# Performance work log

Measured on AMD Instinct MI355X. Metric: run time of the kernel, lower is better.

The kernel has to match this reference:

```python
import jax, jax.numpy as jnp
import numpy as np

EPS = 1e-3  # keras BatchNormalization default epsilon
NUM_HEADS = 8


def conv1d_same(x, w, b):
    # x: [B,T,Cin], w: [K,Cin,Cout]
    return jax.lax.conv_general_dilated(
        x, w, window_strides=(1,), padding='SAME',
        dimension_numbers=('NWC', 'WIO', 'NWC')) + b


def bn(x, g, b, m, v):
    # inference-mode batchnorm with moving stats
    return (x - m) * jax.lax.rsqrt(v + EPS) * g + b


def lstm(x, K, R, b):
    # x: [B,T,D] -> [B,T,U]; keras gate order i,f,c,o; recurrent_dropout off at inference
    B = x.shape[0]
    U = R.shape[0]
    xp = jnp.einsum('btd,dz->btz', x, K) + b  # precompute input projection

    def step(carry, xt):
        h, c = carry
        z = xt + h @ R
        i, f, g, o = jnp.split(z, 4, axis=-1)
        c = jax.nn.sigmoid(f) * c + jax.nn.sigmoid(i) * jnp.tanh(g)
        h = jax.nn.sigmoid(o) * jnp.tanh(c)
        return (h, c), h

    h0 = jnp.zeros((B, U), x.dtype)
    _, hs = jax.lax.scan(step, (h0, h0), jnp.swapaxes(xp, 0, 1))
    return jnp.swapaxes(hs, 0, 1)


def bilstm(x, Kf, Rf, bf, Kb, Rb, bb):
    fwd = lstm(x, Kf, Rf, bf)
    bwd = lstm(x[:, ::-1], Kb, Rb, bb)[:, ::-1]
    return jnp.concatenate([fwd, bwd], axis=-1)


def mhsa(x, wq, bq, wk, bk, wv, bv, wo, bo):
    B, T, _ = x.shape
    d_model = wq.shape[1]
    dh = d_model // NUM_HEADS
    q = (x @ wq + bq).reshape(B, T, NUM_HEADS, dh)
    k = (x @ wk + bk).reshape(B, T, NUM_HEADS, dh)
    v = (x @ wv + bv).reshape(B, T, NUM_HEADS, dh)
    logits = jnp.einsum('bqhd,bkhd->bhqk', q, k) / jnp.sqrt(jnp.asarray(dh, x.dtype))
    attn = jax.nn.softmax(logits, axis=-1)
    out = jnp.einsum('bhqk,bkhd->bqhd', attn, v).reshape(B, T, d_model)
    return out @ wo + bo


def setup_inputs() -> dict:
    key = jax.random.key(0)
    ks = iter(jax.random.split(key, 64))

    def nrm(shape, s=0.05):
        return (jax.random.normal(next(ks), shape) * s).astype(jnp.float32)

    p = {}
    p['x'] = jax.random.normal(next(ks), (512, 256, 78), dtype=jnp.float32)
    for name, shp in [
            ('conv5_w', (5, 78, 64)), ('conv7_w', (7, 78, 64)), ('conv9_w', (9, 78, 64)),
            ('fuse_w', (1, 192, 128)), ('se_w1', (128, 8)), ('se_w2', (8, 128)),
            ('l1f_k', (128, 512)), ('l1f_r', (128, 512)), ('l1b_k', (128, 512)), ('l1b_r', (128, 512)),
            ('l2f_k', (256, 256)), ('l2f_r', (64, 256)), ('l2b_k', (256, 256)), ('l2b_r', (64, 256)),
            ('wq', (128, 256)), ('wk', (128, 256)), ('wv', (128, 256)), ('wo', (256, 256)),
            ('d1_w', (256, 256)), ('d2_w', (256, 128)), ('d3_w', (128, 1)),
            ('conv5_b', (64,)), ('conv7_b', (64,)), ('conv9_b', (64,)), ('fuse_b', (128,)),
            ('se_b1', (8,)), ('se_b2', (128,)),
            ('l1f_b', (512,)), ('l1b_b', (512,)), ('l2f_b', (256,)), ('l2b_b', (256,)),
            ('bq', (256,)), ('bk', (256,)), ('bv', (256,)), ('bo', (256,)),
            ('d1_b', (256,)), ('d2_b', (128,)), ('d3_b', (1,))]:
        p[name] = nrm(shp)
    for tag, c in [('bn5', 64), ('bn7', 64), ('bn9', 64), ('bn_l1', 256),
                   ('bn_l2', 128), ('bn_d1', 256), ('bn_d2', 128)]:
        p[tag + '_g'] = jnp.ones((c,), jnp.float32)
        p[tag + '_b'] = jnp.zeros((c,), jnp.float32)
        p[tag + '_m'] = jnp.zeros((c,), jnp.float32)
        p[tag + '_v'] = jnp.ones((c,), jnp.float32)
    return p


def reference(x, conv5_w, conv5_b, bn5_g, bn5_b, bn5_m, bn5_v,
              conv7_w, conv7_b, bn7_g, bn7_b, bn7_m, bn7_v,
              conv9_w, conv9_b, bn9_g, bn9_b, bn9_m, bn9_v,
              fuse_w, fuse_b, se_w1, se_b1, se_w2, se_b2,
              l1f_k, l1f_r, l1f_b, l1b_k, l1b_r, l1b_b,
              bn_l1_g, bn_l1_b, bn_l1_m, bn_l1_v,
              l2f_k, l2f_r, l2f_b, l2b_k, l2b_r, l2b_b,
              bn_l2_g, bn_l2_b, bn_l2_m, bn_l2_v,
              wq, bq, wk, bk, wv, bv, wo, bo,
              d1_w, d1_b, bn_d1_g, bn_d1_b, bn_d1_m, bn_d1_v,
              d2_w, d2_b, bn_d2_g, bn_d2_b, bn_d2_m, bn_d2_v,
              d3_w, d3_b):
    def block(w, b, g, bt, m, v):
        h = jax.nn.relu(conv1d_same(x, w, b))
        h = bn(h, g, bt, m, v)
        B, T, C = h.shape  # MaxPooling1D(2, 'same'); T is even
        return h.reshape(B, T // 2, 2, C).max(axis=2)

    fused = jnp.concatenate([
        block(conv5_w, conv5_b, bn5_g, bn5_b, bn5_m, bn5_v),
        block(conv7_w, conv7_b, bn7_g, bn7_b, bn7_m, bn7_v),
        block(conv9_w, conv9_b, bn9_g, bn9_b, bn9_m, bn9_v)], axis=-1)
    fused = conv1d_same(fused, fuse_w, fuse_b)

    # SENet spatial attention
    s = fused.mean(axis=1)
    e = jax.nn.sigmoid(jax.nn.relu(s @ se_w1 + se_b1) @ se_w2 + se_b2)
    h = fused * e[:, None, :]

    h = bilstm(h, l1f_k, l1f_r, l1f_b, l1b_k, l1b_r, l1b_b)
    h = bn(h, bn_l1_g, bn_l1_b, bn_l1_m, bn_l1_v)
    h = bilstm(h, l2f_k, l2f_r, l2f_b, l2b_k, l2b_r, l2b_b)
    h = bn(h, bn_l2_g, bn_l2_b, bn_l2_m, bn_l2_v)

    h = mhsa(h, wq, bq, wk, bk, wv, bv, wo, bo)
    g_ = h.mean(axis=1)

    d = jax.nn.relu(g_ @ d1_w + d1_b)
    d = bn(d, bn_d1_g, bn_d1_b, bn_d1_m, bn_d1_v)
    d = jax.nn.relu(d @ d2_w + d2_b)
    d = bn(d, bn_d2_g, bn_d2_b, bn_d2_m, bn_d2_v)
    return jax.nn.sigmoid(d @ d3_w + d3_b)
```

## Files before the change

### kernel.cpp

```cpp
#include <hip/hip_runtime.h>

#define EPS 1e-3f

typedef __attribute__((ext_vector_type(8))) short bf16x8;
typedef __attribute__((ext_vector_type(4))) float f32x4;

__device__ __forceinline__ float sigm(float x){ return 1.0f/(1.0f + __expf(-x)); }
__device__ __forceinline__ float tanhfast(float x){ return 1.0f - 2.0f/(1.0f + __expf(2.0f*x)); }

__device__ __forceinline__ unsigned short f2b(float f){
    union { float f; unsigned u; } v; v.f = f;
    unsigned r = v.u + 0x7FFFu + ((v.u >> 16) & 1u);
    return (unsigned short)(r >> 16);
}
__device__ __forceinline__ float b2f(unsigned short h){
    union { unsigned u; float f; } v; v.u = ((unsigned)h) << 16; return v.f;
}

__global__ void __launch_bounds__(256)
prep_x(const float* __restrict__ x, unsigned short* __restrict__ xbf)
{
    const int b = blockIdx.x;
    const float* xs = x + (size_t)b*256*78;
    unsigned short* xd = xbf + (size_t)b*264*96;
    for (int p = threadIdx.x; p < 264*48; p += 256){
        int row = p / 48;
        int cp  = (p - row*48) * 2;
        int t   = row - 4;
        unsigned short v0 = 0, v1 = 0;
        if (t >= 0 && t < 256){
            if (cp   < 78) v0 = f2b(xs[t*78 + cp]);
            if (cp+1 < 78) v1 = f2b(xs[t*78 + cp + 1]);
        }
        *(unsigned int*)(xd + row*96 + cp) = (unsigned)v0 | ((unsigned)v1 << 16);
    }
}

__global__ void __launch_bounds__(256)
prep_w(const float* __restrict__ w5, const float* __restrict__ w7, const float* __restrict__ w9,
       unsigned short* __restrict__ wfrag)
{
    int g = blockIdx.x*256 + threadIdx.x;
    if (g >= 27*12*64) return;
    union { unsigned short s[8]; uint4 v; } u;
    int base = g * 8;
    #pragma unroll
    for (int e = 0; e < 8; ++e){
        int lin  = base + e;
        int slot = lin & 511;
        int fi   = lin >> 9;
        int nt   = fi % 12, kcs = fi / 12;
        int k    = kcs / 3, cs = kcs - k*3;
        int l15  = slot >> 5, r = slot & 31;
        int lg   = r >> 3, ee = r & 7;
        int ci   = cs*32 + lg*8 + ee;
        int co   = nt*16 + l15;
        float val = 0.f;
        if (ci < 78){
            if (co < 64){
                int kk = k - 2;
                if (kk >= 0 && kk < 5) val = w5[(kk*78 + ci)*64 + co];
            } else if (co < 128){
                int kk = k - 1;
                if (kk >= 0 && kk < 7) val = w7[(kk*78 + ci)*64 + (co - 64)];
            } else {
                val = w9[(k*78 + ci)*64 + (co - 128)];
            }
        }
        u.s[e] = f2b(val);
    }
    *(uint4*)(wfrag + base) = u.v;
}

__global__ void prep_ss(const float* b5, const float* b7, const float* b9,
                        const float* g5, const float* be5, const float* m5, const float* v5,
                        const float* g7, const float* be7, const float* m7, const float* v7,
                        const float* g9, const float* be9, const float* m9, const float* v9,
                        float* __restrict__ biascat, float* __restrict__ scale, float* __restrict__ shift)
{
    int c = threadIdx.x;
    if (c >= 192) return;
    float bv, g, be, m, v;
    if (c < 64){        bv=b5[c];      g=g5[c];      be=be5[c];      m=m5[c];      v=v5[c]; }
    else if (c < 128){  int i=c-64;  bv=b7[i]; g=g7[i]; be=be7[i]; m=m7[i]; v=v7[i]; }
    else {              int i=c-128; bv=b9[i]; g=g9[i]; be=be9[i]; m=m9[i]; v=v9[i]; }
    float s = g * rsqrtf(v + EPS);
    biascat[c] = bv;
    scale[c]   = s;
    shift[c]   = be - m*s;
}

__global__ void __launch_bounds__(256)
conv_mfma(const unsigned short* __restrict__ xbf,
          const unsigned short* __restrict__ wfrag,
          const float* __restrict__ biascat, const float* __restrict__ scale,
          const float* __restrict__ shift,
          float* __restrict__ out)
{
    const int b = blockIdx.x, tile = blockIdx.y;
    const int tid = threadIdx.x, lane = tid & 63, wv = tid >> 6;
    const int l15 = lane & 15, lg = lane >> 4;
    const int nt0 = wv * 3;
    const int t0  = tile * 64;

    f32x4 acc[4][3];
    #pragma unroll
    for (int nt = 0; nt < 3; ++nt){
        float bv = biascat[(nt0 + nt)*16 + l15];
        #pragma unroll
        for (int mt = 0; mt < 4; ++mt)
            acc[mt][nt] = (f32x4){bv, bv, bv, bv};
    }

    const unsigned short* xb = xbf + ((size_t)b*264 + t0 + l15)*96 + lg*8;
    const unsigned short* wb = wfrag + (size_t)nt0*512 + l15*32 + lg*8;

    for (int k = 0; k < 9; ++k){
        #pragma unroll
        for (int cs = 0; cs < 3; ++cs){
            bf16x8 A[4], Bf[3];
            #pragma unroll
            for (int mt = 0; mt < 4; ++mt)
                A[mt] = *(const bf16x8*)(xb + (size_t)(k + mt*16)*96 + cs*32);
            #pragma unroll
            for (int nt = 0; nt < 3; ++nt)
                Bf[nt] = *(const bf16x8*)(wb + (size_t)((k*3 + cs)*12 + nt)*512);
            #pragma unroll
            for (int mt = 0; mt < 4; ++mt)
                #pragma unroll
                for (int nt = 0; nt < 3; ++nt)
                    acc[mt][nt] = __builtin_amdgcn_mfma_f32_16x16x32_bf16(A[mt], Bf[nt], acc[mt][nt], 0, 0, 0);
        }
    }

    #pragma unroll
    for (int nt = 0; nt < 3; ++nt){
        int col = (nt0 + nt)*16 + l15;
        float s = scale[col], sh = shift[col];
        #pragma unroll
        for (int mt = 0; mt < 4; ++mt){
            float v0 = fmaxf(acc[mt][nt][0], 0.f)*s + sh;
            float v1 = fmaxf(acc[mt][nt][1], 0.f)*s + sh;
            float v2 = fmaxf(acc[mt][nt][2], 0.f)*s + sh;
            float v3 = fmaxf(acc[mt][nt][3], 0.f)*s + sh;
            int tb = tile*32 + mt*8 + lg*2;
            out[((size_t)b*128 + tb    )*192 + col] = fmaxf(v0, v1);
            out[((size_t)b*128 + tb + 1)*192 + col] = fmaxf(v2, v3);
        }
    }
}

__global__ void __launch_bounds__(128)
se_mean(const unsigned short* __restrict__ fb,
        const float* __restrict__ w1, const float* __restrict__ b1,
        const float* __restrict__ w2, const float* __restrict__ b2,
        float* __restrict__ e)
{
    int b = blockIdx.x, c = threadIdx.x;
    __shared__ float sv[128];
    __shared__ float rv[8];
    const unsigned short* fp = fb + (size_t)b*128*128 + c;
    float acc = 0.f;
    for (int t = 0; t < 128; ++t) acc += b2f(fp[t*128]);
    sv[c] = acc * (1.f/128.f);
    __syncthreads();
    if (c < 8){
        float r = b1[c];
        for (int i = 0; i < 128; ++i) r = fmaf(sv[i], w1[i*8 + c], r);
        rv[c] = fmaxf(r, 0.f);
    }
    __syncthreads();
    float ev = b2[c];
    #pragma unroll
    for (int j = 0; j < 8; ++j) ev = fmaf(rv[j], w2[j*128 + c], ev);
    e[(size_t)b*128 + c] = sigm(ev);
}

template<int K, bool ABF16, int OUTMODE, bool ESCALE>
__global__ void __launch_bounds__(256)
xp_gemm(const void* __restrict__ Av, const float* __restrict__ W,
        const float* __restrict__ bias, const float* __restrict__ esc,
        unsigned short* __restrict__ outp, int N)
{
    __shared__ unsigned short Asm[128][40];
    __shared__ unsigned short Bsm[8][64][8];
    __shared__ float esm[ESCALE ? K : 1];

    const int tid  = threadIdx.x;
    const int lane = tid & 63;
    const int wv   = tid >> 6;
    const int wm   = wv & 1;
    const int wn   = wv >> 1;
    const size_t m0 = (size_t)blockIdx.x * 128;
    const int n0   = blockIdx.y * 128;

    if constexpr (ESCALE){
        for (int i = tid; i < K; i += 256) esm[i] = esc[(size_t)blockIdx.x*K + i];
    }

    f32x4 acc[4][4];
    #pragma unroll
    for (int nt = 0; nt < 4; ++nt){
        float bv = bias[n0 + wn*64 + nt*16 + (lane & 15)];
        #pragma unroll
        for (int mt = 0; mt < 4; ++mt)
            acc[mt][nt] = (f32x4){bv, bv, bv, bv};
    }

    const int bn = tid & 127;
    const int bg = tid >> 7;

    for (int k0 = 0; k0 < K; k0 += 32){
        __syncthreads();
        if constexpr (!ABF16){
            const float* Ag = (const float*)Av;
            #pragma unroll
            for (int i = 0; i < 2; ++i){
                int g = tid + i*256;
                int r = g >> 2, c8 = g & 3;
                float4 d0 = *(const float4*)(Ag + (m0 + r)*K + k0 + c8*8);
                float4 d1 = *(const float4*)(Ag + (m0 + r)*K + k0 + c8*8 + 4);
                union { unsigned short s[8]; uint4 v; } u;
                u.s[0]=f2b(d0.x); u.s[1]=f2b(d0.y); u.s[2]=f2b(d0.z); u.s[3]=f2b(d0.w);
                u.s[4]=f2b(d1.x); u.s[5]=f2b(d1.y); u.s[6]=f2b(d1.z); u.s[7]=f2b(d1.w);
                *(uint4*)&Asm[r][c8*8] = u.v;
            }
        } else {
            const unsigned short* Ag = (const unsigned short*)Av;
            #pragma unroll
            for (int i = 0; i < 2; ++i){
                int g = tid + i*256;
                int r = g >> 2, c8 = g & 3;
                uint4 d = *(const uint4*)(Ag + (m0 + r)*K + k0 + c8*8);
                if constexpr (ESCALE){
                    unsigned short* s = (unsigned short*)&d;
                    #pragma unroll
                    for (int j = 0; j < 8; ++j)
                        s[j] = f2b(b2f(s[j]) * esm[k0 + c8*8 + j]);
                }
                *(uint4*)&Asm[r][c8*8] = d;
            }
        }
        {
            union { unsigned short s[8]; uint4 v; } u0, u1;
            #pragma unroll
            for (int q = 0; q < 8; ++q){
                u0.s[q] = f2b(W[(size_t)(k0 + bg*16 + q)*N + n0 + bn]);
                u1.s[q] = f2b(W[(size_t)(k0 + bg*16 + 8 + q)*N + n0 + bn]);
            }
            int nt = bn >> 4, lo = bn & 15;
            *(uint4*)&Bsm[nt][lo + 16*(2*bg)][0]   = u0.v;
            *(uint4*)&Bsm[nt][lo + 16*(2*bg+1)][0] = u1.v;
        }
        __syncthreads();

        bf16x8 af[4], bfr[4];
        #pragma unroll
        for (int mt = 0; mt < 4; ++mt)
            af[mt] = *(const bf16x8*)&Asm[wm*64 + mt*16 + (lane & 15)][(lane >> 4)*8];
        #pragma unroll
        for (int nt = 0; nt < 4; ++nt)
            bfr[nt] = *(const bf16x8*)&Bsm[wn*4 + nt][lane][0];
        #pragma unroll
        for (int mt = 0; mt < 4; ++mt)
            #pragma unroll
            for (int nt = 0; nt < 4; ++nt)
                acc[mt][nt] = __builtin_amdgcn_mfma_f32_16x16x32_bf16(af[mt], bfr[nt], acc[mt][nt], 0, 0, 0);
    }

    #pragma unroll
    for (int mt = 0; mt < 4; ++mt)
        #pragma unroll
        for (int nt = 0; nt < 4; ++nt)
            #pragma unroll
            for (int r = 0; r < 4; ++r){
                size_t row = m0 + wm*64 + mt*16 + (lane >> 4)*4 + r;
                int    col = n0 + wn*64 + nt*16 + (lane & 15);
                if constexpr (OUTMODE == 0){
                    outp[row*N + col] = f2b(acc[mt][nt][r]);
                } else if constexpr (OUTMODE == 1){
                    size_t off = ((size_t)((row >> 7)*8 + (col >> 5))*32 + (col & 31))*128 + (row & 127);
                    outp[off] = f2b(acc[mt][nt][r]);
                } else {
                    const int U = N/4;
                    outp[row*N + (col & (U-1))*4 + (col / U)] = f2b(acc[mt][nt][r]);
                }
            }
}

template<int U>
__global__ void __launch_bounds__(4*U)
lstm_rec5(const unsigned short* __restrict__ xpf, const unsigned short* __restrict__ xpb,
          const float* __restrict__ Rf, const float* __restrict__ Rb,
          const float* __restrict__ bng, const float* __restrict__ bnb,
          const float* __restrict__ bnm, const float* __restrict__ bnv,
          unsigned short* __restrict__ outv)
{
    constexpr int Z  = 4*U;
    constexpr int KT = U/32;
    constexpr int HP = U + 8;

    __shared__ unsigned short h_lds[2][16][HP];

    const int tid = threadIdx.x, lane = tid & 63, wv = tid >> 6;
    const int l15 = lane & 15, lg = lane >> 4;
    const int dir = blockIdx.y;
    const int b0  = blockIdx.x * 16;

    const unsigned short* xp = dir ? xpb : xpf;
    const float* Rg = dir ? Rb : Rf;

    for (int i = tid; i < 2*16*HP; i += 4*U) ((unsigned short*)h_lds)[i] = 0;

    bf16x8 rf[KT][4];
    #pragma unroll
    for (int kt = 0; kt < KT; ++kt)
        #pragma unroll
        for (int g = 0; g < 4; ++g){
            union { unsigned short s[8]; bf16x8 v; } u;
            #pragma unroll
            for (int e = 0; e < 8; ++e)
                u.s[e] = f2b(Rg[(size_t)(kt*32 + lg*8 + e)*Z + g*U + wv*16 + l15]);
            rf[kt][g] = u.v;
        }

    const int u_ = wv*16 + l15;
    const int ch = dir*U + u_;
    const float bns  = bng[ch] * rsqrtf(bnv[ch] + EPS);
    const float bnsh = bnb[ch] - bnm[ch]*bns;
    float cst[4] = {0.f, 0.f, 0.f, 0.f};
    const unsigned short* xbase = xp + ((size_t)(b0 + lg*4)*128)*Z + u_*4;

    ushort4 xq[4];
    {
        const int tf = dir ? 127 : 0;
        #pragma unroll
        for (int r = 0; r < 4; ++r)
            xq[r] = *(const ushort4*)(xbase + ((size_t)r*128 + tf)*Z);
    }
    __syncthreads();

    int buf = 0;
    for (int ts = 0; ts < 128; ++ts){
        const int t = dir ? 127 - ts : ts;
        ushort4 xn[4] = {};
        if (ts < 127){
            const int tn = dir ? t - 1 : t + 1;
            #pragma unroll
            for (int r = 0; r < 4; ++r)
                xn[r] = *(const ushort4*)(xbase + ((size_t)r*128 + tn)*Z);
        }
        bf16x8 af[KT];
        #pragma unroll
        for (int kt = 0; kt < KT; ++kt)
            af[kt] = *(const bf16x8*)&h_lds[buf][l15][kt*32 + lg*8];
        f32x4 acc[4];
        #pragma unroll
        for (int g = 0; g < 4; ++g) acc[g] = (f32x4){0.f,0.f,0.f,0.f};
        #pragma unroll
        for (int kt = 0; kt < KT; ++kt)
            #pragma unroll
            for (int g = 0; g < 4; ++g)
                acc[g] = __builtin_amdgcn_mfma_f32_16x16x32_bf16(af[kt], rf[kt][g], acc[g], 0, 0, 0);
        #pragma unroll
        for (int r = 0; r < 4; ++r){
            float zi = acc[0][r] + b2f(xq[r].x);
            float zf = acc[1][r] + b2f(xq[r].y);
            float zg = acc[2][r] + b2f(xq[r].z);
            float zo = acc[3][r] + b2f(xq[r].w);
            float c  = sigm(zf)*cst[r] + sigm(zi)*tanhfast(zg);
            cst[r] = c;
            float h = sigm(zo)*tanhfast(c);
            h_lds[buf^1][lg*4 + r][u_] = f2b(h);
            size_t oidx = ((size_t)(b0 + lg*4 + r)*128 + t)*(size_t)(2*U) + ch;
            outv[oidx] = f2b(fmaf(h, bns, bnsh));
        }
        asm volatile("s_waitcnt lgkmcnt(0)" ::: "memory");
        __builtin_amdgcn_s_barrier();
        buf ^= 1;
        #pragma unroll
        for (int r = 0; r < 4; ++r) xq[r] = xn[r];
    }
}

__global__ void __launch_bounds__(256)
attn_kernel(const unsigned short* __restrict__ qb,
            const unsigned short* __restrict__ kb,
            const unsigned short* __restrict__ vb,
            float* __restrict__ msum)
{
    __shared__ unsigned short p_lds[128][136];
    __shared__ float red[4][2][16];

    const int b  = blockIdx.x, hd = blockIdx.y;
    const int tid = threadIdx.x, lane = tid & 63, wv = tid >> 6;
    const int m0 = wv * 32;
    const int l15 = lane & 15, lg = lane >> 4;

    bf16x8 aq[2];
    #pragma unroll
    for (int mt = 0; mt < 2; ++mt)
        aq[mt] = *(const bf16x8*)(qb + ((size_t)(b*128 + m0 + mt*16 + l15))*256 + hd*32 + lg*8);

    bf16x8 bk[8];
    #pragma unroll
    for (int nt = 0; nt < 8; ++nt)
        bk[nt] = *(const bf16x8*)(kb + ((size_t)(b*128 + nt*16 + l15))*256 + hd*32 + lg*8);

    f32x4 s[2][8];
    #pragma unroll
    for (int mt = 0; mt < 2; ++mt)
        #pragma unroll
        for (int nt = 0; nt < 8; ++nt) s[mt][nt] = (f32x4){0.f,0.f,0.f,0.f};
    #pragma unroll
    for (int mt = 0; mt < 2; ++mt)
        #pragma unroll
        for (int nt = 0; nt < 8; ++nt)
            s[mt][nt] = __builtin_amdgcn_mfma_f32_16x16x32_bf16(aq[mt], bk[nt], s[mt][nt], 0, 0, 0);

    const float scale = 0.17677669529663687f;
    #pragma unroll
    for (int mt = 0; mt < 2; ++mt)
        #pragma unroll
        for (int r = 0; r < 4; ++r){
            float mx = -1e30f;
            #pragma unroll
            for (int nt = 0; nt < 8; ++nt) mx = fmaxf(mx, s[mt][nt][r]);
            #pragma unroll
            for (int msk = 1; msk < 16; msk <<= 1) mx = fmaxf(mx, __shfl_xor(mx, msk, 64));
            float pv[8], sum = 0.f;
            #pragma unroll
            for (int nt = 0; nt < 8; ++nt){
                pv[nt] = __expf((s[mt][nt][r] - mx) * scale);
                sum += pv[nt];
            }
            #pragma unroll
            for (int msk = 1; msk < 16; msk <<= 1) sum += __shfl_xor(sum, msk, 64);
            float inv = 1.f / sum;
            int row = m0 + mt*16 + lg*4 + r;
            #pragma unroll
            for (int nt = 0; nt < 8; ++nt)
                p_lds[row][nt*16 + l15] = f2b(pv[nt] * inv);
        }
    __syncthreads();

    f32x4 o[2][2];
    #pragma unroll
    for (int mt = 0; mt < 2; ++mt)
        #pragma unroll
        for (int dn = 0; dn < 2; ++dn) o[mt][dn] = (f32x4){0.f,0.f,0.f,0.f};
    bf16x8 bv[4][2];
    #pragma unroll
    for (int kt = 0; kt < 4; ++kt)
        #pragma unroll
        for (int dn = 0; dn < 2; ++dn)
            bv[kt][dn] = *(const bf16x8*)(vb + ((size_t)(b*8 + hd)*32 + dn*16 + l15)*128 + kt*32 + lg*8);
    #pragma unroll
    for (int mt = 0; mt < 2; ++mt)
        #pragma unroll
        for (int kt = 0; kt < 4; ++kt){
            bf16x8 ap = *(const bf16x8*)&p_lds[m0 + mt*16 + l15][kt*32 + lg*8];
            #pragma unroll
            for (int dn = 0; dn < 2; ++dn)
                o[mt][dn] = __builtin_amdgcn_mfma_f32_16x16x32_bf16(ap, bv[kt][dn], o[mt][dn], 0, 0, 0);
        }

    float sm[2];
    #pragma unroll
    for (int dn = 0; dn < 2; ++dn){
        float a = 0.f;
        #pragma unroll
        for (int mt = 0; mt < 2; ++mt)
            #pragma unroll
            for (int r = 0; r < 4; ++r) a += o[mt][dn][r];
        a += __shfl_xor(a, 16, 64);
        a += __shfl_xor(a, 32, 64);
        sm[dn] = a;
    }
    if (lg == 0){
        red[wv][0][l15] = sm[0];
        red[wv][1][l15] = sm[1];
    }
    __syncthreads();
    if (tid < 32){
        int dn = tid >> 4, n = tid & 15;
        float tot = red[0][dn][n] + red[1][dn][n] + red[2][dn][n] + red[3][dn][n];
        msum[(size_t)b*256 + hd*32 + dn*16 + n] = tot * (1.f/128.f);
    }
}

__global__ void __launch_bounds__(256)
head_kernel(const float* __restrict__ msum,
            const float* __restrict__ wo, const float* __restrict__ bo,
            const float* __restrict__ d1w, const float* __restrict__ d1b,
            const float* __restrict__ g1, const float* __restrict__ b1,
            const float* __restrict__ m1, const float* __restrict__ v1,
            const float* __restrict__ d2w, const float* __restrict__ d2b,
            const float* __restrict__ g2, const float* __restrict__ b2,
            const float* __restrict__ m2, const float* __restrict__ v2,
            const float* __restrict__ d3w, const float* __restrict__ d3b,
            float* __restrict__ outp)
{
    int b = blockIdx.x, j = threadIdx.x;
    __shared__ float s1[256];
    __shared__ float s2[256];
    const float* mr = msum + (size_t)b*256;
    float acc = bo[j];
    #pragma unroll 4
    for (int i = 0; i < 256; ++i) acc = fmaf(mr[i], wo[i*256 + j], acc);
    s1[j] = acc;
    __syncthreads();
    float a1 = d1b[j];
    #pragma unroll 4
    for (int i = 0; i < 256; ++i) a1 = fmaf(s1[i], d1w[i*256 + j], a1);
    a1 = fmaxf(a1, 0.f);
    float sc1 = g1[j] * rsqrtf(v1[j] + EPS);
    a1 = a1 * sc1 + (b1[j] - m1[j] * sc1);
    s2[j] = a1;
    __syncthreads();
    if (j < 128){
        float a2 = d2b[j];
        #pragma unroll 4
        for (int i = 0; i < 256; ++i) a2 = fmaf(s2[i], d2w[i*128 + j], a2);
        a2 = fmaxf(a2, 0.f);
        float sc2 = g2[j] * rsqrtf(v2[j] + EPS);
        a2 = a2 * sc2 + (b2[j] - m2[j] * sc2);
        s1[j] = a2;
    }
    __syncthreads();
    if (j == 0){
        float a3 = d3b[0];
        for (int i = 0; i < 128; ++i) a3 = fmaf(s1[i], d3w[i], a3);
        outp[b] = sigm(a3);
    }
}

extern "C" void kernel_launch(void* const* d_in, const int* in_sizes, int n_in,
                              void* d_out, int out_size, void* d_ws, size_t ws_size,
                              hipStream_t stream)
{
    #define F(i) ((const float*)d_in[i])
    const float* x       = F(0);
    const float* conv5_w = F(1);
    const float* conv7_w = F(2);
    const float* conv9_w = F(3);
    const float* fuse_w  = F(4);
    const float* se_w1   = F(5);
    const float* se_w2   = F(6);
    const float* l1f_k   = F(7);
    const float* l1f_r   = F(8);
    const float* l1b_k   = F(9);
    const float* l1b_r   = F(10);
    const float* l2f_k   = F(11);
    const float* l2f_r   = F(12);
    const float* l2b_k   = F(13);
    const float* l2b_r   = F(14);
    const float* wq      = F(15);
    const float* wk      = F(16);
    const float* wv      = F(17);
    const float* wo      = F(18);
    const float* d1_w    = F(19);
    const float* d2_w    = F(20);
    const float* d3_w    = F(21);
    const float* conv5_b = F(22);
    const float* conv7_b = F(23);
    const float* conv9_b = F(24);
    const float* fuse_b  = F(25);
    const float* se_b1   = F(26);
    const float* se_b2   = F(27);
    const float* l1f_b   = F(28);
    const float* l1b_b   = F(29);
    const float* l2f_b   = F(30);
    const float* l2b_b   = F(31);
    const float* bq      = F(32);
    const float* bk      = F(33);
    const float* bv      = F(34);
    const float* bo      = F(35);
    const float* d1_b    = F(36);
    const float* d2_b    = F(37);
    const float* d3_b    = F(38);
    const float* bn5_g = F(39), *bn5_b = F(40), *bn5_m = F(41), *bn5_v = F(42);
    const float* bn7_g = F(43), *bn7_b = F(44), *bn7_m = F(45), *bn7_v = F(46);
    const float* bn9_g = F(47), *bn9_b = F(48), *bn9_m = F(49), *bn9_v = F(50);
    const float* bnl1_g = F(51), *bnl1_b = F(52), *bnl1_m = F(53), *bnl1_v = F(54);
    const float* bnl2_g = F(55), *bnl2_b = F(56), *bnl2_m = F(57), *bnl2_v = F(58);
    const float* bnd1_g = F(59), *bnd1_b = F(60), *bnd1_m = F(61), *bnd1_v = F(62);
    const float* bnd2_g = F(63), *bnd2_b = F(64), *bnd2_m = F(65), *bnd2_v = F(66);
    #undef F

    float* ws = (float*)d_ws;
    float* concat = ws;
    unsigned short* fusedbf = (unsigned short*)(ws + 12582912);
    float* e      = ws + 16777216;
    unsigned short* xbf   = (unsigned short*)(ws + 20971520);
    unsigned short* wfrag = (unsigned short*)(ws + 27607040);
    float* biascat = ws + 27689984;
    float* cscale  = ws + 27690176;
    float* cshift  = ws + 27690368;
    unsigned short* xp1f  = (unsigned short*)(ws);
    unsigned short* xp1b  = (unsigned short*)(ws + 20971520);
    unsigned short* l1out = (unsigned short*)(ws + 29360128);
    unsigned short* xp2f  = (unsigned short*)(ws);
    unsigned short* xp2b  = (unsigned short*)(ws + 4194304);
    unsigned short* l2out = (unsigned short*)(ws + 8388608);
    unsigned short* qbuf  = (unsigned short*)(ws + 12582912);
    unsigned short* kbuf  = (unsigned short*)(ws);
    unsigned short* vbuf  = (unsigned short*)(ws + 20971520);
    float* msum   = ws + 29360128;
    float* outp   = (float*)d_out;

    prep_x<<<dim3(512), dim3(256), 0, stream>>>(x, xbf);
    prep_w<<<dim3(81), dim3(256), 0, stream>>>(conv5_w, conv7_w, conv9_w, wfrag);
    prep_ss<<<dim3(1), dim3(192), 0, stream>>>(
        conv5_b, conv7_b, conv9_b,
        bn5_g, bn5_b, bn5_m, bn5_v,
        bn7_g, bn7_b, bn7_m, bn7_v,
        bn9_g, bn9_b, bn9_m, bn9_v,
        biascat, cscale, cshift);
    conv_mfma<<<dim3(512,4), dim3(256), 0, stream>>>(
        xbf, wfrag, biascat, cscale, cshift, concat);

    xp_gemm<192,false,0,false><<<dim3(512,1), dim3(256), 0, stream>>>(
        concat, fuse_w, fuse_b, nullptr, fusedbf, 128);
    se_mean<<<dim3(512), dim3(128), 0, stream>>>(fusedbf, se_w1, se_b1, se_w2, se_b2, e);

    xp_gemm<128,true,2,true><<<dim3(512,4), dim3(256), 0, stream>>>(
        fusedbf, l1f_k, l1f_b, e, xp1f, 512);
    xp_gemm<128,true,2,true><<<dim3(512,4), dim3(256), 0, stream>>>(
        fusedbf, l1b_k, l1b_b, e, xp1b, 512);
    lstm_rec5<128><<<dim3(32,2), dim3(512), 0, stream>>>(
        xp1f, xp1b, l1f_r, l1b_r, bnl1_g, bnl1_b, bnl1_m, bnl1_v, l1out);

    xp_gemm<256,true,2,false><<<dim3(512,2), dim3(256), 0, stream>>>(
        l1out, l2f_k, l2f_b, nullptr, xp2f, 256);
    xp_gemm<256,true,2,false><<<dim3(512,2), dim3(256), 0, stream>>>(
        l1out, l2b_k, l2b_b, nullptr, xp2b, 256);
    lstm_rec5<64><<<dim3(32,2), dim3(256), 0, stream>>>(
        xp2f, xp2b, l2f_r, l2b_r, bnl2_g, bnl2_b, bnl2_m, bnl2_v, l2out);

    xp_gemm<128,true,0,false><<<dim3(512,2), dim3(256), 0, stream>>>(
        l2out, wq, bq, nullptr, qbuf, 256);
    xp_gemm<128,true,0,false><<<dim3(512,2), dim3(256), 0, stream>>>(
        l2out, wk, bk, nullptr, kbuf, 256);
    xp_gemm<128,true,1,false><<<dim3(512,2), dim3(256), 0, stream>>>(
        l2out, wv, bv, nullptr, vbuf, 256);

    attn_kernel<<<dim3(512,8), dim3(256), 0, stream>>>(qbuf, kbuf, vbuf, msum);

    head_kernel<<<dim3(512), dim3(256), 0, stream>>>(
        msum, wo, bo,
        d1_w, d1_b, bnd1_g, bnd1_b, bnd1_m, bnd1_v,
        d2_w, d2_b, bnd2_g, bnd2_b, bnd2_m, bnd2_v,
        d3_w, d3_b, outp);

    (void)in_sizes; (void)n_in; (void)out_size; (void)ws_size;
}
```

Baseline: 862.6 us.

## Prepack GEMM weights to bf16 fragments, batch projection GEMMs, merge LSTM directions

Measured after the change: 1.197 ms. 38.8% more time.

```diff
diff --git a/kernel.cpp b/kernel.cpp
--- a/kernel.cpp
+++ b/kernel.cpp
@@ -72,6 +72,24 @@
     *(uint4*)(wfrag + base) = u.v;
 }
 
+__global__ void __launch_bounds__(256)
+prep_wb(const float* __restrict__ W, unsigned short* __restrict__ dst, int K, int N)
+{
+    int idx = blockIdx.x*256 + threadIdx.x;
+    int NT = N >> 4;
+    int total = (K >> 5) * NT * 64;
+    if (idx >= total) return;
+    int l   = idx & 63;
+    int rem = idx >> 6;
+    int ntg = rem % NT;
+    int ks  = rem / NT;
+    union { unsigned short s[8]; uint4 v; } u;
+    #pragma unroll
+    for (int e = 0; e < 8; ++e)
+        u.s[e] = f2b(W[(size_t)(ks*32 + (l>>4)*8 + e)*N + ntg*16 + (l&15)]);
+    *(uint4*)(dst + (size_t)idx*8) = u.v;
+}
+
 __global__ void prep_ss(const float* b5, const float* b7, const float* b9,
                         const float* g5, const float* be5, const float* m5, const float* v5,
                         const float* g7, const float* be7, const float* m7, const float* v7,
@@ -176,42 +194,37 @@
     e[(size_t)b*128 + c] = sigm(ev);
 }
 
-template<int K, bool ABF16, int OUTMODE, bool ESCALE>
+template<int K, bool ABF16, bool ESCALE>
 __global__ void __launch_bounds__(256)
-xp_gemm(const void* __restrict__ Av, const float* __restrict__ W,
-        const float* __restrict__ bias, const float* __restrict__ esc,
-        unsigned short* __restrict__ outp, int N)
-{
-    __shared__ unsigned short Asm[128][40];
-    __shared__ unsigned short Bsm[8][64][8];
+xp_gemm2(const void* __restrict__ Av,
+         const unsigned short* __restrict__ W0, const unsigned short* __restrict__ W1, const unsigned short* __restrict__ W2,
+         const float* __restrict__ b0p, const float* __restrict__ b1p, const float* __restrict__ b2p,
+         unsigned short* __restrict__ o0, unsigned short* __restrict__ o1, unsigned short* __restrict__ o2,
+         const float* __restrict__ esc,
+         int N, int yper, int om0, int om1, int om2)
+{
+    constexpr int KS = K/32;
+    __shared__ unsigned short Asm[2][128][40];
     __shared__ float esm[ESCALE ? K : 1];
 
-    const int tid  = threadIdx.x;
-    const int lane = tid & 63;
-    const int wv   = tid >> 6;
-    const int wm   = wv & 1;
-    const int wn   = wv >> 1;
+    const int tid = threadIdx.x, lane = tid & 63, wv = tid >> 6;
+    const int wm = wv & 1, wn = wv >> 1;
     const size_t m0 = (size_t)blockIdx.x * 128;
-    const int n0   = blockIdx.y * 128;
+    const int sel = blockIdx.y / yper;
+    const int n0  = (blockIdx.y - sel*yper) * 128;
+    const unsigned short* W = (sel == 0) ? W0 : (sel == 1 ? W1 : W2);
+    const float* bias       = (sel == 0) ? b0p : (sel == 1 ? b1p : b2p);
+    unsigned short* outp    = (sel == 0) ? o0 : (sel == 1 ? o1 : o2);
+    const int om            = (sel == 0) ? om0 : (sel == 1 ? om1 : om2);
+    const int NTf = N >> 4;
 
     if constexpr (ESCALE){
         for (int i = tid; i < K; i += 256) esm[i] = esc[(size_t)blockIdx.x*K + i];
-    }
-
-    f32x4 acc[4][4];
-    #pragma unroll
-    for (int nt = 0; nt < 4; ++nt){
-        float bv = bias[n0 + wn*64 + nt*16 + (lane & 15)];
-        #pragma unroll
-        for (int mt = 0; mt < 4; ++mt)
-            acc[mt][nt] = (f32x4){bv, bv, bv, bv};
-    }
-
-    const int bn = tid & 127;
-    const int bg = tid >> 7;
-
-    for (int k0 = 0; k0 < K; k0 += 32){
         __syncthreads();
+    }
+
+    auto stage = [&](int bq, int ksl){
+        const int k0 = ksl*32;
         if constexpr (!ABF16){
             const float* Ag = (const float*)Av;
             #pragma unroll
@@ -223,7 +236,7 @@
                 union { unsigned short s[8]; uint4 v; } u;
                 u.s[0]=f2b(d0.x); u.s[1]=f2b(d0.y); u.s[2]=f2b(d0.z); u.s[3]=f2b(d0.w);
                 u.s[4]=f2b(d1.x); u.s[5]=f2b(d1.y); u.s[6]=f2b(d1.z); u.s[7]=f2b(d1.w);
-                *(uint4*)&Asm[r][c8*8] = u.v;
+                *(uint4*)&Asm[bq][r][c8*8] = u.v;
             }
         } else {
             const unsigned short* Ag = (const unsigned short*)Av;
@@ -238,36 +251,46 @@
                     for (int j = 0; j < 8; ++j)
                         s[j] = f2b(b2f(s[j]) * esm[k0 + c8*8 + j]);
                 }
-                *(uint4*)&Asm[r][c8*8] = d;
+                *(uint4*)&Asm[bq][r][c8*8] = d;
             }
         }
-        {
-            union { unsigned short s[8]; uint4 v; } u0, u1;
-            #pragma unroll
-            for (int q = 0; q < 8; ++q){
-                u0.s[q] = f2b(W[(size_t)(k0 + bg*16 + q)*N + n0 + bn]);
-                u1.s[q] = f2b(W[(size_t)(k0 + bg*16 + 8 + q)*N + n0 + bn]);
-            }
-            int nt = bn >> 4, lo = bn & 15;
-            *(uint4*)&Bsm[nt][lo + 16*(2*bg)][0]   = u0.v;
-            *(uint4*)&Bsm[nt][lo + 16*(2*bg+1)][0] = u1.v;
-        }
-        __syncthreads();
+    };
+
+    f32x4 acc[4][4];
+    #pragma unroll
+    for (int nt = 0; nt < 4; ++nt){
+        float bv = bias[n0 + wn*64 + nt*16 + (lane & 15)];
+        #pragma unroll
+        for (int mt = 0; mt < 4; ++mt)
+            acc[mt][nt] = (f32x4){bv, bv, bv, bv};
+    }
+
+    stage(0, 0);
+    __syncthreads();
+
+    int buf = 0;
+    for (int ks = 0; ks < KS; ++ks){
+        if (ks + 1 < KS) stage(buf ^ 1, ks + 1);
 
         bf16x8 af[4], bfr[4];
         #pragma unroll
         for (int mt = 0; mt < 4; ++mt)
-            af[mt] = *(const bf16x8*)&Asm[wm*64 + mt*16 + (lane & 15)][(lane >> 4)*8];
-        #pragma unroll
-        for (int nt = 0; nt < 4; ++nt)
-            bfr[nt] = *(const bf16x8*)&Bsm[wn*4 + nt][lane][0];
+            af[mt] = *(const bf16x8*)&Asm[buf][wm*64 + mt*16 + (lane & 15)][(lane >> 4)*8];
+        #pragma unroll
+        for (int nt = 0; nt < 4; ++nt){
+            int ntg = (n0 >> 4) + wn*4 + nt;
+            bfr[nt] = *(const bf16x8*)(W + ((size_t)(ks*NTf + ntg)*64 + lane)*8);
+        }
         #pragma unroll
         for (int mt = 0; mt < 4; ++mt)
             #pragma unroll
             for (int nt = 0; nt < 4; ++nt)
                 acc[mt][nt] = __builtin_amdgcn_mfma_f32_16x16x32_bf16(af[mt], bfr[nt], acc[mt][nt], 0, 0, 0);
-    }
-
+        __syncthreads();
+        buf ^= 1;
+    }
+
+    const int Uq = N >> 2;
     #pragma unroll
     for (int mt = 0; mt < 4; ++mt)
         #pragma unroll
@@ -276,41 +299,43 @@
             for (int r = 0; r < 4; ++r){
                 size_t row = m0 + wm*64 + mt*16 + (lane >> 4)*4 + r;
                 int    col = n0 + wn*64 + nt*16 + (lane & 15);
-                if constexpr (OUTMODE == 0){
-                    outp[row*N + col] = f2b(acc[mt][nt][r]);
-                } else if constexpr (OUTMODE == 1){
+                unsigned short val = f2b(acc[mt][nt][r]);
+                if (om == 0){
+                    outp[row*N + col] = val;
+                } else if (om == 1){
                     size_t off = ((size_t)((row >> 7)*8 + (col >> 5))*32 + (col & 31))*128 + (row & 127);
-                    outp[off] = f2b(acc[mt][nt][r]);
+                    outp[off] = val;
                 } else {
-                    const int U = N/4;
-                    outp[row*N + (col & (U-1))*4 + (col / U)] = f2b(acc[mt][nt][r]);
+                    outp[row*N + (col & (Uq-1))*4 + (col / Uq)] = val;
                 }
             }
 }
 
 template<int U>
-__global__ void __launch_bounds__(4*U)
-lstm_rec5(const unsigned short* __restrict__ xpf, const unsigned short* __restrict__ xpb,
+__global__ void __launch_bounds__(8*U)
+lstm_rec6(const unsigned short* __restrict__ xpf, const unsigned short* __restrict__ xpb,
           const float* __restrict__ Rf, const float* __restrict__ Rb,
           const float* __restrict__ bng, const float* __restrict__ bnb,
           const float* __restrict__ bnm, const float* __restrict__ bnv,
           unsigned short* __restrict__ outv)
 {
-    constexpr int Z  = 4*U;
-    constexpr int KT = U/32;
-    constexpr int HP = U + 8;
-
-    __shared__ unsigned short h_lds[2][16][HP];
+    constexpr int Z   = 4*U;
+    constexpr int KT  = U/32;
+    constexpr int HP  = U + 8;
+    constexpr int WPD = U/16;
+
+    __shared__ unsigned short h_lds[2][2][16][HP];
 
     const int tid = threadIdx.x, lane = tid & 63, wv = tid >> 6;
     const int l15 = lane & 15, lg = lane >> 4;
-    const int dir = blockIdx.y;
+    const int dir = wv / WPD;
+    const int wvl = wv - dir*WPD;
     const int b0  = blockIdx.x * 16;
 
     const unsigned short* xp = dir ? xpb : xpf;
     const float* Rg = dir ? Rb : Rf;
 
-    for (int i = tid; i < 2*16*HP; i += 4*U) ((unsigned short*)h_lds)[i] = 0;
+    for (int i = tid; i < 2*2*16*HP; i += 8*U) ((unsigned short*)h_lds)[i] = 0;
 
     bf16x8 rf[KT][4];
     #pragma unroll
@@ -320,11 +345,11 @@
             union { unsigned short s[8]; bf16x8 v; } u;
             #pragma unroll
             for (int e = 0; e < 8; ++e)
-                u.s[e] = f2b(Rg[(size_t)(kt*32 + lg*8 + e)*Z + g*U + wv*16 + l15]);
+                u.s[e] = f2b(Rg[(size_t)(kt*32 + lg*8 + e)*Z + g*U + wvl*16 + l15]);
             rf[kt][g] = u.v;
         }
 
-    const int u_ = wv*16 + l15;
+    const int u_ = wvl*16 + l15;
     const int ch = dir*U + u_;
     const float bns  = bng[ch] * rsqrtf(bnv[ch] + EPS);
     const float bnsh = bnb[ch] - bnm[ch]*bns;
@@ -353,7 +378,7 @@
         bf16x8 af[KT];
         #pragma unroll
         for (int kt = 0; kt < KT; ++kt)
-            af[kt] = *(const bf16x8*)&h_lds[buf][l15][kt*32 + lg*8];
+            af[kt] = *(const bf16x8*)&h_lds[dir][buf][l15][kt*32 + lg*8];
         f32x4 acc[4];
         #pragma unroll
         for (int g = 0; g < 4; ++g) acc[g] = (f32x4){0.f,0.f,0.f,0.f};
@@ -371,12 +396,11 @@
             float c  = sigm(zf)*cst[r] + sigm(zi)*tanhfast(zg);
             cst[r] = c;
             float h = sigm(zo)*tanhfast(c);
-            h_lds[buf^1][lg*4 + r][u_] = f2b(h);
+            h_lds[dir][buf^1][lg*4 + r][u_] = f2b(h);
             size_t oidx = ((size_t)(b0 + lg*4 + r)*128 + t)*(size_t)(2*U) + ch;
             outv[oidx] = f2b(fmaf(h, bns, bnsh));
         }
-        asm volatile("s_waitcnt lgkmcnt(0)" ::: "memory");
-        __builtin_amdgcn_s_barrier();
+        __syncthreads();
         buf ^= 1;
         #pragma unroll
         for (int r = 0; r < 4; ++r) xq[r] = xn[r];
@@ -589,24 +613,33 @@
     #undef F
 
     float* ws = (float*)d_ws;
-    float* concat = ws;
-    unsigned short* fusedbf = (unsigned short*)(ws + 12582912);
-    float* e      = ws + 16777216;
-    unsigned short* xbf   = (unsigned short*)(ws + 20971520);
-    unsigned short* wfrag = (unsigned short*)(ws + 27607040);
-    float* biascat = ws + 27689984;
-    float* cscale  = ws + 27690176;
-    float* cshift  = ws + 27690368;
+    unsigned short* wbB = (unsigned short*)(ws + 37556224);
+    unsigned short* l1fkb = wbB;
+    unsigned short* l1bkb = wbB + 65536;
+    unsigned short* l2fkb = wbB + 131072;
+    unsigned short* l2bkb = wbB + 196608;
+    unsigned short* wqb   = wbB + 262144;
+    unsigned short* wkb   = wbB + 294912;
+    unsigned short* wvb   = wbB + 327680;
+    unsigned short* fusewb= wbB + 360448;
+    unsigned short* xbf   = (unsigned short*)(ws);
+    unsigned short* wfrag = (unsigned short*)(ws + 6488064);
+    float* biascat = ws + 6529536;
+    float* cscale  = ws + 6529728;
+    float* cshift  = ws + 6529920;
+    float* concat  = ws + 6530112;
+    unsigned short* fusedbf = (unsigned short*)(ws + 19113024);
+    float* e       = ws + 21210176;
     unsigned short* xp1f  = (unsigned short*)(ws);
-    unsigned short* xp1b  = (unsigned short*)(ws + 20971520);
-    unsigned short* l1out = (unsigned short*)(ws + 29360128);
+    unsigned short* xp1b  = (unsigned short*)(ws + 8388608);
+    unsigned short* l1out = (unsigned short*)(ws + 21275712);
     unsigned short* xp2f  = (unsigned short*)(ws);
-    unsigned short* xp2b  = (unsigned short*)(ws + 4194304);
-    unsigned short* l2out = (unsigned short*)(ws + 8388608);
-    unsigned short* qbuf  = (unsigned short*)(ws + 12582912);
-    unsigned short* kbuf  = (unsigned short*)(ws);
-    unsigned short* vbuf  = (unsigned short*)(ws + 20971520);
-    float* msum   = ws + 29360128;
+    unsigned short* xp2b  = (unsigned short*)(ws + 2097152);
+    unsigned short* l2out = (unsigned short*)(ws + 4194304);
+    unsigned short* qbuf  = (unsigned short*)(ws + 8388608);
+    unsigned short* kbuf  = (unsigned short*)(ws + 16777216);
+    unsigned short* vbuf  = (unsigned short*)(ws + 25165824);
+    float* msum   = ws;
     float* outp   = (float*)d_out;
 
     prep_x<<<dim3(512), dim3(256), 0, stream>>>(x, xbf);
@@ -617,36 +650,39 @@
         bn7_g, bn7_b, bn7_m, bn7_v,
         bn9_g, bn9_b, bn9_m, bn9_v,
         biascat, cscale, cshift);
+    prep_wb<<<dim3(32), dim3(256), 0, stream>>>(l1f_k, l1fkb, 128, 512);
+    prep_wb<<<dim3(32), dim3(256), 0, stream>>>(l1b_k, l1bkb, 128, 512);
+    prep_wb<<<dim3(32), dim3(256), 0, stream>>>(l2f_k, l2fkb, 256, 256);
+    prep_wb<<<dim3(32), dim3(256), 0, stream>>>(l2b_k, l2bkb, 256, 256);
+    prep_wb<<<dim3(16), dim3(256), 0, stream>>>(wq, wqb, 128, 256);
+    prep_wb<<<dim3(16), dim3(256), 0, stream>>>(wk, wkb, 128, 256);
+    prep_wb<<<dim3(16), dim3(256), 0, stream>>>(wv, wvb, 128, 256);
+    prep_wb<<<dim3(12), dim3(256), 0, stream>>>(fuse_w, fusewb, 192, 128);
+
     conv_mfma<<<dim3(512,4), dim3(256), 0, stream>>>(
         xbf, wfrag, biascat, cscale, cshift, concat);
-
-    xp_gemm<192,false,0,false><<<dim3(512,1), dim3(256), 0, stream>>>(
-        concat, fuse_w, fuse_b, nullptr, fusedbf, 128);
+    xp_gemm2<192,false,false><<<dim3(512,1), dim3(256), 0, stream>>>(
+        concat, fusewb, fusewb, fusewb, fuse_b, fuse_b, fuse_b,
+        fusedbf, fusedbf, fusedbf, nullptr, 128, 1, 0, 0, 0);
     se_mean<<<dim3(512), dim3(128), 0, stream>>>(fusedbf, se_w1, se_b1, se_w2, se_b2, e);
 
-    xp_gemm<128,true,2,true><<<dim3(512,4), dim3(256), 0, stream>>>(
-        fusedbf, l1f_k, l1f_b, e, xp1f, 512);
-    xp_gemm<128,true,2,true><<<dim3(512,4), dim3(256), 0, stream>>>(
-        fusedbf, l1b_k, l1b_b, e, xp1b, 512);
-    lstm_rec5<128><<<dim3(32,2), dim3(512), 0, stream>>>(
+    xp_gemm2<128,true,true><<<dim3(512,8), dim3(256), 0, stream>>>(
+        fusedbf, l1fkb, l1bkb, l1bkb, l1f_b, l1b_b, l1b_b,
+        xp1f, xp1b, xp1b, e, 512, 4, 2, 2, 2);
+    lstm_rec6<128><<<dim3(32), dim3(1024), 0, stream>>>(
         xp1f, xp1b, l1f_r, l1b_r, bnl1_g, bnl1_b, bnl1_m, bnl1_v, l1out);
 
-    xp_gemm<256,true,2,false><<<dim3(512,2), dim3(256), 0, stream>>>(
-        l1out, l2f_k, l2f_b, nullptr, xp2f, 256);
-    xp_gemm<256,true,2,false><<<dim3(512,2), dim3(256), 0, stream>>>(
-        l1out, l2b_k, l2b_b, nullptr, xp2b, 256);
-    lstm_rec5<64><<<dim3(32,2), dim3(256), 0, stream>>>(
+    xp_gemm2<256,true,false><<<dim3(512,4), dim3(256), 0, stream>>>(
+        l1out, l2fkb, l2bkb, l2bkb, l2f_b, l2b_b, l2b_b,
+        xp2f, xp2b, xp2b, nullptr, 256, 2, 2, 2, 2);
+    lstm_rec6<64><<<dim3(32), dim3(512), 0, stream>>>(
         xp2f, xp2b, l2f_r, l2b_r, bnl2_g, bnl2_b, bnl2_m, bnl2_v, l2out);
 
-    xp_gemm<128,true,0,false><<<dim3(512,2), dim3(256), 0, stream>>>(
-        l2out, wq, bq, nullptr, qbuf, 256);
-    xp_gemm<128,true,0,false><<<dim3(512,2), dim3(256), 0, stream>>>(
-        l2out, wk, bk, nullptr, kbuf, 256);
-    xp_gemm<128,true,1,false><<<dim3(512,2), dim3(256), 0, stream>>>(
-        l2out, wv, bv, nullptr, vbuf, 256);
+    xp_gemm2<128,true,false><<<dim3(512,6), dim3(256), 0, stream>>>(
+        l2out, wqb, wkb, wvb, bq, bk, bv,
+        qbuf, kbuf, vbuf, nullptr, 256, 2, 0, 0, 1);
 
     attn_kernel<<<dim3(512,8), dim3(256), 0, stream>>>(qbuf, kbuf, vbuf, msum);
-
     head_kernel<<<dim3(512), dim3(256), 0, stream>>>(
         msum, wo, bo,
         d1_w, d1_b, bnd1_g, bnd1_b, bnd1_m, bnd1_v,
```
